# Kernel optimization log

Measured on AMD Instinct MI355X. Metric: run time of the kernel, lower is better.

The kernel has to match this reference:

```python
import jax, jax.numpy as jnp
import numpy as np

GROUPS = 32
EPS = 1e-5

def group_norm(x, scale, bias):
    b, c, h, w = x.shape
    xg = x.reshape(b, GROUPS, c // GROUPS, h, w)
    mean = xg.mean(axis=(2, 3, 4), keepdims=True)
    var = xg.var(axis=(2, 3, 4), keepdims=True)
    xg = (xg - mean) * jax.lax.rsqrt(var + EPS)
    x = xg.reshape(b, c, h, w)
    return x * scale[None, :, None, None] + bias[None, :, None, None]

def conv2d(x, w, b, pad):
    y = jax.lax.conv_general_dilated(
        x, w, window_strides=(1, 1), padding=[(pad, pad), (pad, pad)],
        dimension_numbers=('NCHW', 'OIHW', 'NCHW'))
    return y + b[None, :, None, None]

def setup_inputs() -> dict:
    key = jax.random.key(0)
    ks = jax.random.split(key, 16)
    B, Cin, Cout, H, W, TDIM, NCON = 4, 128, 128, 64, 64, 512, 4
    s = 0.05
    return {
        'x': jax.random.normal(ks[0], (B, Cin, H, W), jnp.float32),
        't': jax.random.normal(ks[1], (B, TDIM), jnp.float32),
        'aim': jax.random.randint(ks[2], (B,), 0, NCON),
        'cond': jax.random.normal(ks[3], (B, Cin, H, W), jnp.float32),
        'gn1_scale': jnp.ones((Cin,), jnp.float32),
        'gn1_bias': jnp.zeros((Cin,), jnp.float32),
        'conv1_w': jax.random.normal(ks[4], (Cout, Cin, 3, 3), jnp.float32) * s,
        'conv1_b': jnp.zeros((Cout,), jnp.float32),
        'mlp_w': jax.random.normal(ks[5], (Cout, TDIM), jnp.float32) * s,
        'mlp_b': jnp.zeros((Cout,), jnp.float32),
        'cond_w': jax.random.normal(ks[6], (Cout, Cin, 1, 1), jnp.float32) * s,
        'cond_b': jnp.zeros((Cout,), jnp.float32),
        'gn2_scale': jnp.ones((Cout,), jnp.float32),
        'gn2_bias': jnp.zeros((Cout,), jnp.float32),
        'conv2_w': jax.random.normal(ks[7], (Cout, Cout, 3, 3), jnp.float32) * s,
        'conv2_b': jnp.zeros((Cout,), jnp.float32),
        'contrast_embed': jax.random.normal(ks[8], (NCON, Cout, 1, 1), jnp.float32),
    }

def reference(x, t, aim, cond, gn1_scale, gn1_bias, conv1_w, conv1_b,
              mlp_w, mlp_b, cond_w, cond_b, gn2_scale, gn2_bias,
              conv2_w, conv2_b, contrast_embed):
    # block1: GN -> SiLU -> 3x3 conv
    h = conv2d(jax.nn.silu(group_norm(x, gn1_scale, gn1_bias)), conv1_w, conv1_b, 1)
    # time embedding: SiLU -> Linear, broadcast over spatial
    temb = jax.nn.silu(t) @ mlp_w.T + mlp_b  # (b, out_ch)
    h = h + temb[:, :, None, None]
    # spatial cross-attention with cond
    c = conv2d(cond, cond_w, cond_b, 0)  # 1x1 projection, (b, C, u, v)
    C = h.shape[1]
    score = jnp.einsum('bchw,bcuv->bhwuv', h, c)  # (b, h, w, u, v)
    # NOTE: softmax over dim=1 (the spatial h axis), as in the source
    score = jax.nn.softmax(score / jnp.sqrt(jnp.float32(C)), axis=1)
    h = h + jnp.einsum('bhwuv,bcuv->bchw', score, c)
    # contrast embedding lookup
    h = h + contrast_embed[aim]  # (b, C, 1, 1) broadcast
    # block2: GN -> SiLU -> (dropout=identity at eval) -> 3x3 conv
    h = conv2d(jax.nn.silu(group_norm(h, gn2_scale, gn2_bias)), conv2_w, conv2_b, 1)
    # res_conv is Identity since in_ch == out_ch
    return h + x
```

## Files before the change

### kernel.cpp

```cpp
#include <hip/hip_runtime.h>
#include <cmath>

#define BB 4
#define CC 128
#define HH 64
#define WW 64
#define SP 4096
#define NG 32
#define TT 64
#define NS 2
#define PSZ ((size_t)BB * SP * CC)

typedef __bf16 bf16x8 __attribute__((ext_vector_type(8)));
typedef __bf16 bf16x4 __attribute__((ext_vector_type(4)));
typedef float  f32x4  __attribute__((ext_vector_type(4)));

__device__ __forceinline__ float silu_f(float v) {
    return v / (1.f + __expf(-v));
}

__device__ __forceinline__ float fast_exp2(float x) {
    return exp2f(x);
}

template<int CTRL>
__device__ __forceinline__ float dpp_add(float v) {
    int m = __builtin_amdgcn_update_dpp(0, __float_as_int(v), CTRL, 0xF, 0xF, true);
    return v + __int_as_float(m);
}
__device__ __forceinline__ float row16_sum(float v) {
    v = dpp_add<0xB1>(v);
    v = dpp_add<0x4E>(v);
    v = dpp_add<0x141>(v);
    v = dpp_add<0x140>(v);
    return v;
}

__global__ __launch_bounds__(256) void prep_kernel(
    const float* __restrict__ x, const float* __restrict__ gn1s,
    const float* __restrict__ gn1b, __bf16* __restrict__ aT,
    const float* __restrict__ c1w, const float* __restrict__ c2w,
    __bf16* __restrict__ wt,
    const float* __restrict__ t, const float* __restrict__ mlpw,
    const float* __restrict__ mlpb, float* __restrict__ tembw,
    const float* __restrict__ cond, const float* __restrict__ cw,
    const float* __restrict__ cb, __bf16* __restrict__ cmT,
    __bf16* __restrict__ cm2, float* __restrict__ gstat)
{
    __shared__ __align__(16) char pool[18432];
    __shared__ float rs[4], rs2[4], mean_s, inv_s;
    const int blk = blockIdx.x;
    const int tid = threadIdx.x;

    if (blk < 128) {
        const int b = blk >> 5, g = blk & 31;
        const float* p = x + (size_t)blk * 16384;
        float s = 0.f, s2 = 0.f;
        for (int it = 0; it < 16; ++it) {
            int q = it * 256 + tid;
            float4 v = *(const float4*)&p[q * 4];
            s += v.x + v.y + v.z + v.w;
            s2 += v.x * v.x + v.y * v.y + v.z * v.z + v.w * v.w;
        }
        #pragma unroll
        for (int off = 32; off >= 1; off >>= 1) {
            s  += __shfl_down(s,  off, 64);
            s2 += __shfl_down(s2, off, 64);
        }
        const int wid = tid >> 6;
        if ((tid & 63) == 0) { rs[wid] = s; rs2[wid] = s2; }
        __syncthreads();
        if (tid == 0) {
            float S = rs[0] + rs[1] + rs[2] + rs[3];
            float S2 = rs2[0] + rs2[1] + rs2[2] + rs2[3];
            float m = S * (1.f / 16384.f);
            float var = S2 * (1.f / 16384.f) - m * m;
            mean_s = m;
            inv_s = rsqrtf(var + 1e-5f);
        }
        __syncthreads();
        const float m = mean_s, inv = inv_s;
        float sc[4], bi[4];
        #pragma unroll
        for (int j = 0; j < 4; ++j) { sc[j] = gn1s[g * 4 + j]; bi[j] = gn1b[g * 4 + j]; }
        for (int it = 0; it < 16; ++it) {
            int pp = it * 256 + tid;
            bf16x4 o;
            #pragma unroll
            for (int j = 0; j < 4; ++j)
                o[j] = (__bf16)silu_f((p[j * 4096 + pp] - m) * inv * sc[j] + bi[j]);
            *(bf16x4*)&aT[((size_t)(b * SP + pp)) * CC + g * 4] = o;
        }
    } else if (blk < 146) {
        const int idx = blk - 128;
        const int wsel = idx / 9, tap = idx % 9;
        const float* src = wsel ? c2w : c1w;
        __bf16* dst = wt + (size_t)wsel * 9 * 16384 + (size_t)tap * 16384;
        for (int it = 0; it < 64; ++it) {
            int q = it * 256 + tid;
            dst[q] = (__bf16)src[(size_t)q * 9 + tap];
        }
    } else if (blk < 154) {
        const int cog = blk - 146;
        float* st = (float*)pool;
        for (int it = 0; it < 8; ++it) {
            int q = it * 256 + tid;
            st[q] = silu_f(t[q]);
        }
        __syncthreads();
        const int col = tid >> 4, seg = tid & 15;
        const float* wr = mlpw + (size_t)(cog * 16 + col) * 512 + seg * 32;
        float acc[4] = {0.f, 0.f, 0.f, 0.f};
        #pragma unroll
        for (int k8 = 0; k8 < 8; ++k8) {
            float4 wv = *(const float4*)&wr[k8 * 4];
            #pragma unroll
            for (int j = 0; j < 4; ++j) {
                int k = seg * 32 + k8 * 4 + j;
                float w4 = (&wv.x)[j];
                acc[0] += st[0 * 512 + k] * w4;
                acc[1] += st[1 * 512 + k] * w4;
                acc[2] += st[2 * 512 + k] * w4;
                acc[3] += st[3 * 512 + k] * w4;
            }
        }
        #pragma unroll
        for (int o = 1; o < 16; o <<= 1) {
            #pragma unroll
            for (int b4 = 0; b4 < 4; ++b4)
                acc[b4] += __shfl_xor(acc[b4], o, 64);
        }
        if (seg == 0) {
            float bv = mlpb[cog * 16 + col];
            #pragma unroll
            for (int b4 = 0; b4 < 4; ++b4)
                tembw[b4 * 128 + cog * 16 + col] = acc[b4] + bv;
        }
    } else if (blk < 410) {
        const int pblk = blk - 154;
        const int b = pblk >> 6;
        const int p0 = (pblk & 63) * 64;
        const int l = tid & 63, wv = tid >> 6;
        const int l15 = l & 15, l4 = l >> 4;
        const int mB = wv * 32;

        __bf16* XT = (__bf16*)pool;

        for (int it = 0; it < 32; ++it) {
            int q = it * 256 + tid;
            float v = cond[((size_t)(b * CC + (q >> 6))) * SP + p0 + (q & 63)];
            XT[(q & 63) * 136 + (q >> 6)] = (__bf16)v;
        }
        __syncthreads();

        f32x4 acc[2][4];
        #pragma unroll
        for (int mb = 0; mb < 2; ++mb)
            #pragma unroll
            for (int nt = 0; nt < 4; ++nt) acc[mb][nt] = (f32x4){0.f, 0.f, 0.f, 0.f};

        #pragma unroll
        for (int ks = 0; ks < 4; ++ks) {
            bf16x8 bfr[4];
            #pragma unroll
            for (int nt = 0; nt < 4; ++nt)
                bfr[nt] = *(const bf16x8*)&XT[(nt * 16 + l15) * 136 + ks * 32 + l4 * 8];
            #pragma unroll
            for (int mb = 0; mb < 2; ++mb) {
                const float* wrow = cw + (size_t)(mB + mb * 16 + l15) * 128 + ks * 32 + l4 * 8;
                float4 wa = *(const float4*)wrow;
                float4 wb4 = *(const float4*)(wrow + 4);
                bf16x8 afr;
                afr[0] = (__bf16)wa.x; afr[1] = (__bf16)wa.y;
                afr[2] = (__bf16)wa.z; afr[3] = (__bf16)wa.w;
                afr[4] = (__bf16)wb4.x; afr[5] = (__bf16)wb4.y;
                afr[6] = (__bf16)wb4.z; afr[7] = (__bf16)wb4.w;
                #pragma unroll
                for (int nt = 0; nt < 4; ++nt)
                    acc[mb][nt] = __builtin_amdgcn_mfma_f32_16x16x32_bf16(afr, bfr[nt], acc[mb][nt], 0, 0, 0);
            }
        }

        const float scl = 0.12751743f;
        #pragma unroll
        for (int mb = 0; mb < 2; ++mb) {
            int co0 = mB + mb * 16 + l4 * 4;
            float bv[4];
            #pragma unroll
            for (int r = 0; r < 4; ++r) bv[r] = cb[co0 + r];
            #pragma unroll
            for (int nt = 0; nt < 4; ++nt) {
                int p = p0 + nt * 16 + l15;
                bf16x4 o;
                #pragma unroll
                for (int r = 0; r < 4; ++r)
                    o[r] = (__bf16)((acc[mb][nt][r] + bv[r]) * scl);
                *(bf16x4*)&cmT[((size_t)(b * SP + p)) * CC + co0] = o;
            }
        }
        __syncthreads();
        __bf16* O2 = (__bf16*)pool;
        #pragma unroll
        for (int mb = 0; mb < 2; ++mb) {
            int co0 = mB + mb * 16 + l4 * 4;
            #pragma unroll
            for (int r = 0; r < 4; ++r) {
                float bv = cb[co0 + r];
                #pragma unroll
                for (int nt = 0; nt < 4; ++nt)
                    O2[(co0 + r) * 72 + nt * 16 + l15] = (__bf16)(acc[mb][nt][r] + bv);
            }
        }
        __syncthreads();
        #pragma unroll
        for (int it = 0; it < 4; ++it) {
            int q = it * 256 + tid;
            int co = q >> 3, pc = q & 7;
            *(bf16x8*)&cm2[((size_t)(b * CC + co)) * SP + p0 + pc * 8] =
                *(const bf16x8*)&O2[co * 72 + pc * 8];
        }
    } else {
        gstat[tid] = 0.f;
    }
}

template<bool FUSE_TEMB, bool OUT_CF, bool FUSE_GN>
__global__ __launch_bounds__(512, 4) void conv_mfma_kernel(
    const __bf16* __restrict__ inT, const __bf16* __restrict__ wt,
    const float* __restrict__ bias, const float* __restrict__ temb,
    const float* __restrict__ resid, __bf16* __restrict__ outT,
    float* __restrict__ outF, const float* __restrict__ gstat,
    const float* __restrict__ gn_s, const float* __restrict__ gn_b)
{
    const int y   = blockIdx.x >> 1;
    const int xh2 = blockIdx.x & 1;
    const int x0  = xh2 * 32;
    const int b   = blockIdx.y;
    const int tid = threadIdx.x;
    const int l = tid & 63, wv = tid >> 6;
    const int l15 = l & 15, l4 = l >> 4;
    const int co_w = wv * 16;

    __shared__ __bf16 inS[3 * 16 * 34 * 8];
    __shared__ float af[128], bfp[128];

    if (FUSE_GN) {
        if (tid < 128) {
            int g = tid >> 2;
            float S = gstat[(b * NG + g) * 2], S2 = gstat[(b * NG + g) * 2 + 1];
            float m = S * (1.f / 16384.f);
            float var = S2 * (1.f / 16384.f) - m * m;
            float inv = rsqrtf(var + 1e-5f);
            float a = inv * gn_s[tid];
            af[tid] = a;
            bfp[tid] = gn_b[tid] - m * a;
        }
        __syncthreads();
    }

    const __bf16* inTb = inT + (size_t)b * SP * CC;
    for (int q = tid; q < 3 * 34 * 16; q += 512) {
        int cc = q & 15;
        int t2 = q >> 4;
        int xs = t2 % 34;
        int r  = t2 / 34;
        int yy = y + r - 1;
        int xg = x0 + xs - 1;
        bf16x8 v;
        if (((unsigned)yy < 64u) && ((unsigned)xg < 64u)) {
            bf16x8 raw = *(const bf16x8*)&inTb[((size_t)(yy * 64 + xg)) * CC + cc * 8];
            if (FUSE_GN) {
                #pragma unroll
                for (int j = 0; j < 8; ++j) {
                    int c = cc * 8 + j;
                    v[j] = (__bf16)silu_f((float)raw[j] * af[c] + bfp[c]);
                }
            } else {
                v = raw;
            }
        } else {
            #pragma unroll
            for (int j = 0; j < 8; ++j) v[j] = (__bf16)0.f;
        }
        *(bf16x8*)&inS[((r * 16 + cc) * 34 + xs) * 8] = v;
    }
    __syncthreads();

    f32x4 acc[2];
    acc[0] = (f32x4){0.f, 0.f, 0.f, 0.f};
    acc[1] = (f32x4){0.f, 0.f, 0.f, 0.f};

    const __bf16* wp = wt + (size_t)(co_w + l15) * 128 + l4 * 8;
    bf16x8 wb[2][4];
    #pragma unroll
    for (int ks = 0; ks < 4; ++ks)
        wb[0][ks] = *(const bf16x8*)(wp + ks * 32);

    #pragma unroll
    for (int tap = 0; tap < 9; ++tap) {
        const int cur = tap & 1, nxt = cur ^ 1;
        if (tap < 8) {
            #pragma unroll
            for (int ks = 0; ks < 4; ++ks)
                wb[nxt][ks] = *(const bf16x8*)(wp + (tap + 1) * 16384 + ks * 32);
        }
        const int rr = tap / 3, dx = tap % 3;
        #pragma unroll
        for (int ks = 0; ks < 4; ++ks) {
            const __bf16* rb = &inS[((rr * 16 + ks * 4 + l4) * 34) * 8];
            bf16x8 b0 = *(const bf16x8*)&rb[(dx + l15) * 8];
            bf16x8 b1 = *(const bf16x8*)&rb[(16 + dx + l15) * 8];
            acc[0] = __builtin_amdgcn_mfma_f32_16x16x32_bf16(wb[cur][ks], b0, acc[0], 0, 0, 0);
            acc[1] = __builtin_amdgcn_mfma_f32_16x16x32_bf16(wb[cur][ks], b1, acc[1], 0, 0, 0);
        }
    }

    if (OUT_CF) {
        #pragma unroll
        for (int r = 0; r < 4; ++r) {
            int co = co_w + l4 * 4 + r;
            float bv = bias[co];
            #pragma unroll
            for (int nb = 0; nb < 2; ++nb) {
                int p = y * 64 + x0 + nb * 16 + l15;
                size_t o = ((size_t)(b * CC + co)) * SP + p;
                outF[o] = acc[nb][r] + bv + resid[o];
            }
        }
    } else {
        int co0 = co_w + l4 * 4;
        float bv[4];
        #pragma unroll
        for (int r = 0; r < 4; ++r)
            bv[r] = bias[co0 + r] + (FUSE_TEMB ? temb[b * CC + co0 + r] : 0.f);
        #pragma unroll
        for (int nb = 0; nb < 2; ++nb) {
            int p = y * 64 + x0 + nb * 16 + l15;
            bf16x4 o;
            #pragma unroll
            for (int r = 0; r < 4; ++r)
                o[r] = (__bf16)(acc[nb][r] + bv[r]);
            *(bf16x4*)&outT[((size_t)(b * SP + p)) * CC + co0] = o;
        }
    }
}

#define CT2 72
#define PBS 72
#define POOL_BYTES 55296
#define NIT (SP / TT / NS)

__global__ __launch_bounds__(512, 4) void attn_kernel(
    const __bf16* __restrict__ h1T, const __bf16* __restrict__ cmT,
    const __bf16* __restrict__ cm2, __bf16* __restrict__ parts)
{
    const int bid = blockIdx.x;
    const int w = bid >> 3;
    const int b = (bid >> 1) & 3;
    const int s = bid & 1;
    const int tid = threadIdx.x;
    const int wid = tid >> 6;
    const int l = tid & 63, l15 = l & 15, l4 = l >> 4;

    __shared__ __align__(16) char pool[POOL_BYTES];
    __bf16* ct2p = (__bf16*)pool;
    __bf16* Pbp  = (__bf16*)(pool + 36864);
    __bf16* Otr  = (__bf16*)pool;

    const __bf16* h1Tb = h1T + (size_t)b * SP * CC;
    const __bf16* cmTb = cmT + (size_t)b * SP * CC;
    const __bf16* cm2b = cm2 + (size_t)b * CC * SP;

    if (wid < 4) {
        const int pw = wid;
        bf16x8 hfr[4][4];
        #pragma unroll
        for (int nt = 0; nt < 4; ++nt)
            #pragma unroll
            for (int ks = 0; ks < 4; ++ks)
                hfr[nt][ks] = *(const bf16x8*)&h1Tb[((size_t)((nt * 16 + l15) * WW + w)) * CC + ks * 32 + l4 * 8];

        bf16x8 afr[4];

        {
            const int uv0 = s * TT;
            const __bf16* arow = cmTb + (size_t)(uv0 + 16 * pw + l15) * CC;
            bf16x8 a0[4];
            #pragma unroll
            for (int ks = 0; ks < 4; ++ks) a0[ks] = *(const bf16x8*)&arow[ks * 32 + l4 * 8];
            f32x4 s1[4];
            __builtin_amdgcn_s_setprio(1);
            #pragma unroll
            for (int nt = 0; nt < 4; ++nt) {
                s1[nt] = (f32x4){0.f, 0.f, 0.f, 0.f};
                #pragma unroll
                for (int ks = 0; ks < 4; ++ks)
                    s1[nt] = __builtin_amdgcn_mfma_f32_16x16x32_bf16(a0[ks], hfr[nt][ks], s1[nt], 0, 0, 0);
            }
            __builtin_amdgcn_s_setprio(0);
            {
                const int uv1 = (NS + s) * TT;
                const __bf16* arow1 = cmTb + (size_t)(uv1 + 16 * pw + l15) * CC;
                #pragma unroll
                for (int ks = 0; ks < 4; ++ks) afr[ks] = *(const bf16x8*)&arow1[ks * 32 + l4 * 8];
            }
            #pragma unroll
            for (int r = 0; r < 4; ++r) {
                float e0 = fast_exp2(s1[0][r]), e1 = fast_exp2(s1[1][r]);
                float e2 = fast_exp2(s1[2][r]), e3 = fast_exp2(s1[3][r]);
                float sm = (e0 + e1) + (e2 + e3);
                sm = row16_sum(sm);
                float ri = 1.f / sm;
                s1[0][r] = e0 * ri; s1[1][r] = e1 * ri;
                s1[2][r] = e2 * ri; s1[3][r] = e3 * ri;
            }
            #pragma unroll
            for (int nt = 0; nt < 4; ++nt) {
                bf16x4 pk;
                pk[0] = (__bf16)s1[nt][0]; pk[1] = (__bf16)s1[nt][1];
                pk[2] = (__bf16)s1[nt][2]; pk[3] = (__bf16)s1[nt][3];
                *(bf16x4*)&Pbp[(nt * 16 + l15) * PBS + 16 * pw + l4 * 4] = pk;
            }
        }
        __syncthreads();

        for (int i = 0; i < NIT; ++i) {
            if (i < NIT - 1) {
                f32x4 s1[4];
                __builtin_amdgcn_s_setprio(1);
                #pragma unroll
                for (int nt = 0; nt < 4; ++nt) {
                    s1[nt] = (f32x4){0.f, 0.f, 0.f, 0.f};
                    #pragma unroll
                    for (int ks = 0; ks < 4; ++ks)
                        s1[nt] = __builtin_amdgcn_mfma_f32_16x16x32_bf16(afr[ks], hfr[nt][ks], s1[nt], 0, 0, 0);
                }
                __builtin_amdgcn_s_setprio(0);
                if (i < NIT - 2) {
                    const int uv2 = ((i + 2) * NS + s) * TT;
                    const __bf16* arow = cmTb + (size_t)(uv2 + 16 * pw + l15) * CC;
                    #pragma unroll
                    for (int ks = 0; ks < 4; ++ks) afr[ks] = *(const bf16x8*)&arow[ks * 32 + l4 * 8];
                }
                #pragma unroll
                for (int r = 0; r < 4; ++r) {
                    float e0 = fast_exp2(s1[0][r]), e1 = fast_exp2(s1[1][r]);
                    float e2 = fast_exp2(s1[2][r]), e3 = fast_exp2(s1[3][r]);
                    float sm = (e0 + e1) + (e2 + e3);
                    sm = row16_sum(sm);
                    float ri = 1.f / sm;
                    s1[0][r] = e0 * ri; s1[1][r] = e1 * ri;
                    s1[2][r] = e2 * ri; s1[3][r] = e3 * ri;
                }
                __bf16* PbW = Pbp + ((i & 1) ^ 1) * 4608;
                #pragma unroll
                for (int nt = 0; nt < 4; ++nt) {
                    bf16x4 pk;
                    pk[0] = (__bf16)s1[nt][0]; pk[1] = (__bf16)s1[nt][1];
                    pk[2] = (__bf16)s1[nt][2]; pk[3] = (__bf16)s1[nt][3];
                    *(bf16x4*)&PbW[(nt * 16 + l15) * PBS + 16 * pw + l4 * 4] = pk;
                }
            }
            __syncthreads();
        }
    } else {
        const int cw = wid - 4;
        const int hB = (cw & 1) * 32;
        const int cB = (cw >> 1) * 64;
        const int tc = tid - 256;
        const int sc = tc >> 3;
        const int stc = tc & 7;

        f32x4 acc2[2][4];
        #pragma unroll
        for (int mb = 0; mb < 2; ++mb)
            #pragma unroll
            for (int nt = 0; nt < 4; ++nt) acc2[mb][nt] = (f32x4){0.f, 0.f, 0.f, 0.f};

        bf16x8 st4[4];

        {
            const int uv0 = s * TT;
            #pragma unroll
            for (int it = 0; it < 4; ++it) {
                int c = it * 32 + sc;
                *(bf16x8*)&ct2p[c * CT2 + stc * 8] =
                    *(const bf16x8*)&cm2b[(size_t)c * SP + uv0 + stc * 8];
            }
            const int uv1 = (NS + s) * TT;
            #pragma unroll
            for (int it = 0; it < 4; ++it) {
                int c = it * 32 + sc;
                st4[it] = *(const bf16x8*)&cm2b[(size_t)c * SP + uv1 + stc * 8];
            }
        }
        __syncthreads();

        for (int i = 0; i < NIT; ++i) {
            const int cur = i & 1;
            {
                const __bf16* PbR = Pbp + cur * 4608;
                const __bf16* ctR = ct2p + cur * 9216;
                bf16x8 pfr[2][2];
                #pragma unroll
                for (int mb = 0; mb < 2; ++mb)
                    #pragma unroll
                    for (int ks = 0; ks < 2; ++ks)
                        pfr[mb][ks] = *(const bf16x8*)&PbR[(hB + mb * 16 + l15) * PBS + ks * 32 + l4 * 8];
                bf16x8 bfr[4][2];
                #pragma unroll
                for (int nt = 0; nt < 4; ++nt)
                    #pragma unroll
                    for (int ks = 0; ks < 2; ++ks)
                        bfr[nt][ks] = *(const bf16x8*)&ctR[(cB + nt * 16 + l15) * CT2 + ks * 32 + l4 * 8];
                __builtin_amdgcn_s_setprio(1);
                #pragma unroll
                for (int mb = 0; mb < 2; ++mb)
                    #pragma unroll
                    for (int nt = 0; nt < 4; ++nt)
                        #pragma unroll
                        for (int ks = 0; ks < 2; ++ks)
                            acc2[mb][nt] = __builtin_amdgcn_mfma_f32_16x16x32_bf16(
                                pfr[mb][ks], bfr[nt][ks], acc2[mb][nt], 0, 0, 0);
                __builtin_amdgcn_s_setprio(0);
            }
            if (i < NIT - 1) {
                __bf16* ctW = ct2p + (cur ^ 1) * 9216;
                #pragma unroll
                for (int it = 0; it < 4; ++it) {
                    int c = it * 32 + sc;
                    *(bf16x8*)&ctW[c * CT2 + stc * 8] = st4[it];
                }
                if (i < NIT - 2) {
                    const int uv2 = ((i + 2) * NS + s) * TT;
                    #pragma unroll
                    for (int it = 0; it < 4; ++it) {
                        int c = it * 32 + sc;
                        st4[it] = *(const bf16x8*)&cm2b[(size_t)c * SP + uv2 + stc * 8];
                    }
                }
            }
            __syncthreads();
        }

        #pragma unroll
        for (int mb = 0; mb < 2; ++mb)
            #pragma unroll
            for (int nt = 0; nt < 4; ++nt)
                #pragma unroll
                for (int r = 0; r < 4; ++r)
                    Otr[(hB + mb * 16 + l4 * 4 + r) * 136 + cB + nt * 16 + l15] =
                        (__bf16)acc2[mb][nt][r];
    }

    __syncthreads();
    __bf16* pO = parts + (size_t)s * PSZ;
    #pragma unroll
    for (int it = 0; it < 2; ++it) {
        int q = it * 512 + tid;
        int h = q >> 4, cc = q & 15;
        *(bf16x8*)&pO[((size_t)(b * SP + h * WW + w)) * CC + cc * 8] =
            *(const bf16x8*)&Otr[h * 136 + cc * 8];
    }
}

__global__ __launch_bounds__(256) void gn2_stats_kernel(
    const __bf16* __restrict__ h1T, const __bf16* __restrict__ parts,
    const int* __restrict__ aim, const float* __restrict__ emb,
    __bf16* __restrict__ h2T, float* __restrict__ gstat)
{
    const int pb = blockIdx.x, b = blockIdx.y;
    const int tid = threadIdx.x;
    const int c8 = tid & 15, rw = tid >> 4;
    const float4 ev0 = *(const float4*)&emb[aim[b] * CC + c8 * 8];
    const float4 ev1 = *(const float4*)&emb[aim[b] * CC + c8 * 8 + 4];
    float sa = 0.f, s2a = 0.f, sb = 0.f, s2b = 0.f;
    #pragma unroll
    for (int it = 0; it < 2; ++it) {
        int prow = pb * 32 + it * 16 + rw;
        size_t base = ((size_t)(b * SP + prow)) * CC + c8 * 8;
        bf16x8 hv = *(const bf16x8*)&h1T[base];
        bf16x8 a0 = *(const bf16x8*)&parts[base];
        bf16x8 a1 = *(const bf16x8*)&parts[PSZ + base];
        float v[8];
        #pragma unroll
        for (int j = 0; j < 4; ++j)
            v[j] = (float)hv[j] + (&ev0.x)[j] + (float)a0[j] + (float)a1[j];
        #pragma unroll
        for (int j = 4; j < 8; ++j)
            v[j] = (float)hv[j] + (&ev1.x)[j - 4] + (float)a0[j] + (float)a1[j];
        bf16x8 o;
        #pragma unroll
        for (int j = 0; j < 8; ++j) o[j] = (__bf16)v[j];
        *(bf16x8*)&h2T[base] = o;
        #pragma unroll
        for (int j = 0; j < 4; ++j) { sa += v[j]; s2a += v[j] * v[j]; }
        #pragma unroll
        for (int j = 4; j < 8; ++j) { sb += v[j]; s2b += v[j] * v[j]; }
    }
    sa  += __shfl_xor(sa,  16, 64); sa  += __shfl_xor(sa,  32, 64);
    s2a += __shfl_xor(s2a, 16, 64); s2a += __shfl_xor(s2a, 32, 64);
    sb  += __shfl_xor(sb,  16, 64); sb  += __shfl_xor(sb,  32, 64);
    s2b += __shfl_xor(s2b, 16, 64); s2b += __shfl_xor(s2b, 32, 64);
    __shared__ float ls[4][16][4];
    const int wv = tid >> 6;
    if ((tid & 63) < 16) {
        ls[wv][c8][0] = sa;  ls[wv][c8][1] = s2a;
        ls[wv][c8][2] = sb;  ls[wv][c8][3] = s2b;
    }
    __syncthreads();
    if (tid < 16) {
        float A = 0.f, A2 = 0.f, Bs = 0.f, B2 = 0.f;
        #pragma unroll
        for (int v2 = 0; v2 < 4; ++v2) {
            A  += ls[v2][tid][0]; A2 += ls[v2][tid][1];
            Bs += ls[v2][tid][2]; B2 += ls[v2][tid][3];
        }
        atomicAdd(&gstat[(b * NG + tid * 2) * 2],     A);
        atomicAdd(&gstat[(b * NG + tid * 2) * 2 + 1], A2);
        atomicAdd(&gstat[(b * NG + tid * 2 + 1) * 2],     Bs);
        atomicAdd(&gstat[(b * NG + tid * 2 + 1) * 2 + 1], B2);
    }
}

extern "C" void kernel_launch(void* const* d_in, const int* in_sizes, int n_in,
                              void* d_out, int out_size, void* d_ws, size_t ws_size,
                              hipStream_t stream)
{
    const float* x     = (const float*)d_in[0];
    const float* t     = (const float*)d_in[1];
    const int*   aim   = (const int*)  d_in[2];
    const float* cond  = (const float*)d_in[3];
    const float* gn1s  = (const float*)d_in[4];
    const float* gn1b  = (const float*)d_in[5];
    const float* c1w   = (const float*)d_in[6];
    const float* c1b   = (const float*)d_in[7];
    const float* mlpw  = (const float*)d_in[8];
    const float* mlpb  = (const float*)d_in[9];
    const float* cw    = (const float*)d_in[10];
    const float* cb    = (const float*)d_in[11];
    const float* gn2s  = (const float*)d_in[12];
    const float* gn2b  = (const float*)d_in[13];
    const float* c2w   = (const float*)d_in[14];
    const float* c2b   = (const float*)d_in[15];
    const float* emb   = (const float*)d_in[16];
    float* out = (float*)d_out;
    float* ws = (float*)d_ws;

    __bf16* aT    = (__bf16*)ws;
    __bf16* h1T   = (__bf16*)(ws + 1048576);
    __bf16* cmT   = (__bf16*)(ws + 2097152);
    __bf16* cm2   = (__bf16*)(ws + 3145728);
    __bf16* parts = (__bf16*)(ws + 4194304);
    __bf16* wt    = (__bf16*)(ws + 6291456);
    float*  tembw = ws + 6438912;
    float*  gstat = ws + 6439424;
    __bf16* h2T   = cmT;

    prep_kernel<<<dim3(411), dim3(256), 0, stream>>>(
        x, gn1s, gn1b, aT, c1w, c2w, wt, t, mlpw, mlpb, tembw,
        cond, cw, cb, cmT, cm2, gstat);
    conv_mfma_kernel<true, false, false><<<dim3(128, BB), dim3(512), 0, stream>>>(
        aT, wt, c1b, tembw, nullptr, h1T, nullptr, nullptr, nullptr, nullptr);
    attn_kernel<<<dim3(WW * BB * NS), dim3(512), 0, stream>>>(h1T, cmT, cm2, parts);
    gn2_stats_kernel<<<dim3(128, BB), dim3(256), 0, stream>>>(h1T, parts, aim, emb, h2T, gstat);
    conv_mfma_kernel<false, true, true><<<dim3(128, BB), dim3(512), 0, stream>>>(
        h2T, wt + (size_t)9 * 16384, c2b, nullptr, x, nullptr, out, gstat, gn2s, gn2b);
}
```

Measured before the change: 215.4 us.

## Fuse split-K attention partial reduction and GN2 stats into attention kernel

Merges the two uv-split halves of each attention column into one 1024-thread block, so the partial outputs stay in LDS and are combined on-chip instead of going through a global parts buffer. The residual add, contrast embedding, h2T write and GN2 group-stat atomics move into the attention epilogue, which removes the separate gn2_stats kernel and its global round trip. The cost is half as many blocks, doubled LDS per block (about 110KB) which lowers occupancy, and block-wide __syncthreads now spanning both split groups.

```diff
diff --git a/kernel.cpp b/kernel.cpp
--- a/kernel.cpp
+++ b/kernel.cpp
@@ -347,32 +347,37 @@
 
 #define CT2 72
 #define PBS 72
-#define POOL_BYTES 55296
+#define PIPE_BYTES 55296
 #define NIT (SP / TT / NS)
 
-__global__ __launch_bounds__(512, 4) void attn_kernel(
+__global__ __launch_bounds__(1024, 4) void attn_kernel(
     const __bf16* __restrict__ h1T, const __bf16* __restrict__ cmT,
-    const __bf16* __restrict__ cm2, __bf16* __restrict__ parts)
+    const __bf16* __restrict__ cm2, __bf16* __restrict__ h2T,
+    const int* __restrict__ aim, const float* __restrict__ emb,
+    float* __restrict__ gstat)
 {
     const int bid = blockIdx.x;
-    const int w = bid >> 3;
-    const int b = (bid >> 1) & 3;
-    const int s = bid & 1;
+    const int b = bid & 3;
+    const int w = bid >> 2;
     const int tid = threadIdx.x;
     const int wid = tid >> 6;
+    const int sg  = wid >> 3;
+    const int wl  = wid & 7;
     const int l = tid & 63, l15 = l & 15, l4 = l >> 4;
-
-    __shared__ __align__(16) char pool[POOL_BYTES];
-    __bf16* ct2p = (__bf16*)pool;
-    __bf16* Pbp  = (__bf16*)(pool + 36864);
-    __bf16* Otr  = (__bf16*)pool;
+    const int s = sg;
+
+    __shared__ __align__(16) char pool[2 * PIPE_BYTES];
+    __shared__ float ls[16][16][4];
+    char* base = pool + sg * PIPE_BYTES;
+    __bf16* ct2p = (__bf16*)base;
+    __bf16* Pbp  = (__bf16*)(base + 36864);
 
     const __bf16* h1Tb = h1T + (size_t)b * SP * CC;
     const __bf16* cmTb = cmT + (size_t)b * SP * CC;
     const __bf16* cm2b = cm2 + (size_t)b * CC * SP;
 
-    if (wid < 4) {
-        const int pw = wid;
+    if (wl < 4) {
+        const int pw = wl;
         bf16x8 hfr[4][4];
         #pragma unroll
         for (int nt = 0; nt < 4; ++nt)
@@ -464,10 +469,10 @@
             __syncthreads();
         }
     } else {
-        const int cw = wid - 4;
+        const int cw = wl - 4;
         const int hB = (cw & 1) * 32;
         const int cB = (cw >> 1) * 64;
-        const int tc = tid - 256;
+        const int tc = tid & 255;
         const int sc = tc >> 3;
         const int stc = tc & 7;
 
@@ -543,6 +548,7 @@
             __syncthreads();
         }
 
+        __bf16* Otr = (__bf16*)base;
         #pragma unroll
         for (int mb = 0; mb < 2; ++mb)
             #pragma unroll
@@ -554,72 +560,50 @@
     }
 
     __syncthreads();
-    __bf16* pO = parts + (size_t)s * PSZ;
-    #pragma unroll
-    for (int it = 0; it < 2; ++it) {
-        int q = it * 512 + tid;
-        int h = q >> 4, cc = q & 15;
-        *(bf16x8*)&pO[((size_t)(b * SP + h * WW + w)) * CC + cc * 8] =
-            *(const bf16x8*)&Otr[h * 136 + cc * 8];
-    }
-}
-
-__global__ __launch_bounds__(256) void gn2_stats_kernel(
-    const __bf16* __restrict__ h1T, const __bf16* __restrict__ parts,
-    const int* __restrict__ aim, const float* __restrict__ emb,
-    __bf16* __restrict__ h2T, float* __restrict__ gstat)
-{
-    const int pb = blockIdx.x, b = blockIdx.y;
-    const int tid = threadIdx.x;
-    const int c8 = tid & 15, rw = tid >> 4;
-    const float4 ev0 = *(const float4*)&emb[aim[b] * CC + c8 * 8];
-    const float4 ev1 = *(const float4*)&emb[aim[b] * CC + c8 * 8 + 4];
-    float sa = 0.f, s2a = 0.f, sb = 0.f, s2b = 0.f;
-    #pragma unroll
-    for (int it = 0; it < 2; ++it) {
-        int prow = pb * 32 + it * 16 + rw;
-        size_t base = ((size_t)(b * SP + prow)) * CC + c8 * 8;
-        bf16x8 hv = *(const bf16x8*)&h1T[base];
-        bf16x8 a0 = *(const bf16x8*)&parts[base];
-        bf16x8 a1 = *(const bf16x8*)&parts[PSZ + base];
+    {
+        const __bf16* Otr0 = (const __bf16*)pool;
+        const __bf16* Otr1 = (const __bf16*)(pool + PIPE_BYTES);
+        const int h = tid >> 4, cc = tid & 15;
+        const int off = h * 136 + cc * 8;
+        bf16x8 o0 = *(const bf16x8*)&Otr0[off];
+        bf16x8 o1 = *(const bf16x8*)&Otr1[off];
+        size_t gbase = ((size_t)(b * SP + h * WW + w)) * CC + cc * 8;
+        bf16x8 hv = *(const bf16x8*)&h1T[gbase];
+        const float4 ev0 = *(const float4*)&emb[aim[b] * CC + cc * 8];
+        const float4 ev1 = *(const float4*)&emb[aim[b] * CC + cc * 8 + 4];
         float v[8];
         #pragma unroll
         for (int j = 0; j < 4; ++j)
-            v[j] = (float)hv[j] + (&ev0.x)[j] + (float)a0[j] + (float)a1[j];
+            v[j] = (float)hv[j] + (float)o0[j] + (float)o1[j] + (&ev0.x)[j];
         #pragma unroll
         for (int j = 4; j < 8; ++j)
-            v[j] = (float)hv[j] + (&ev1.x)[j - 4] + (float)a0[j] + (float)a1[j];
-        bf16x8 o;
-        #pragma unroll
-        for (int j = 0; j < 8; ++j) o[j] = (__bf16)v[j];
-        *(bf16x8*)&h2T[base] = o;
+            v[j] = (float)hv[j] + (float)o0[j] + (float)o1[j] + (&ev1.x)[j - 4];
+        bf16x8 ov;
+        #pragma unroll
+        for (int j = 0; j < 8; ++j) ov[j] = (__bf16)v[j];
+        *(bf16x8*)&h2T[gbase] = ov;
+        float sa = 0.f, s2a = 0.f, sb = 0.f, s2b = 0.f;
         #pragma unroll
         for (int j = 0; j < 4; ++j) { sa += v[j]; s2a += v[j] * v[j]; }
         #pragma unroll
         for (int j = 4; j < 8; ++j) { sb += v[j]; s2b += v[j] * v[j]; }
-    }
-    sa  += __shfl_xor(sa,  16, 64); sa  += __shfl_xor(sa,  32, 64);
-    s2a += __shfl_xor(s2a, 16, 64); s2a += __shfl_xor(s2a, 32, 64);
-    sb  += __shfl_xor(sb,  16, 64); sb  += __shfl_xor(sb,  32, 64);
-    s2b += __shfl_xor(s2b, 16, 64); s2b += __shfl_xor(s2b, 32, 64);
-    __shared__ float ls[4][16][4];
-    const int wv = tid >> 6;
-    if ((tid & 63) < 16) {
-        ls[wv][c8][0] = sa;  ls[wv][c8][1] = s2a;
-        ls[wv][c8][2] = sb;  ls[wv][c8][3] = s2b;
+        sa  += __shfl_xor(sa,  16, 64); sa  += __shfl_xor(sa,  32, 64);
+        s2a += __shfl_xor(s2a, 16, 64); s2a += __shfl_xor(s2a, 32, 64);
+        sb  += __shfl_xor(sb,  16, 64); sb  += __shfl_xor(sb,  32, 64);
+        s2b += __shfl_xor(s2b, 16, 64); s2b += __shfl_xor(s2b, 32, 64);
+        if (l < 16) {
+            ls[wid][l][0] = sa;  ls[wid][l][1] = s2a;
+            ls[wid][l][2] = sb;  ls[wid][l][3] = s2b;
+        }
     }
     __syncthreads();
-    if (tid < 16) {
-        float A = 0.f, A2 = 0.f, Bs = 0.f, B2 = 0.f;
-        #pragma unroll
-        for (int v2 = 0; v2 < 4; ++v2) {
-            A  += ls[v2][tid][0]; A2 += ls[v2][tid][1];
-            Bs += ls[v2][tid][2]; B2 += ls[v2][tid][3];
-        }
-        atomicAdd(&gstat[(b * NG + tid * 2) * 2],     A);
-        atomicAdd(&gstat[(b * NG + tid * 2) * 2 + 1], A2);
-        atomicAdd(&gstat[(b * NG + tid * 2 + 1) * 2],     Bs);
-        atomicAdd(&gstat[(b * NG + tid * 2 + 1) * 2 + 1], B2);
+    if (tid < 64) {
+        const int cc = tid & 15, k = tid >> 4;
+        float v = 0.f;
+        #pragma unroll
+        for (int wv = 0; wv < 16; ++wv) v += ls[wv][cc][k];
+        const int g = cc * 2 + (k >> 1);
+        atomicAdd(&gstat[(b * NG + g) * 2 + (k & 1)], v);
     }
 }
 
@@ -651,19 +635,18 @@
     __bf16* h1T   = (__bf16*)(ws + 1048576);
     __bf16* cmT   = (__bf16*)(ws + 2097152);
     __bf16* cm2   = (__bf16*)(ws + 3145728);
-    __bf16* parts = (__bf16*)(ws + 4194304);
+    __bf16* h2T   = (__bf16*)(ws + 4194304);
     __bf16* wt    = (__bf16*)(ws + 6291456);
     float*  tembw = ws + 6438912;
     float*  gstat = ws + 6439424;
-    __bf16* h2T   = cmT;
 
     prep_kernel<<<dim3(411), dim3(256), 0, stream>>>(
         x, gn1s, gn1b, aT, c1w, c2w, wt, t, mlpw, mlpb, tembw,
         cond, cw, cb, cmT, cm2, gstat);
     conv_mfma_kernel<true, false, false><<<dim3(128, BB), dim3(512), 0, stream>>>(
         aT, wt, c1b, tembw, nullptr, h1T, nullptr, nullptr, nullptr, nullptr);
-    attn_kernel<<<dim3(WW * BB * NS), dim3(512), 0, stream>>>(h1T, cmT, cm2, parts);
-    gn2_stats_kernel<<<dim3(128, BB), dim3(256), 0, stream>>>(h1T, parts, aim, emb, h2T, gstat);
+    attn_kernel<<<dim3(WW * BB), dim3(1024), 0, stream>>>(
+        h1T, cmT, cm2, h2T, aim, emb, gstat);
     conv_mfma_kernel<false, true, true><<<dim3(128, BB), dim3(512), 0, stream>>>(
         h2T, wt + (size_t)9 * 16384, c2b, nullptr, x, nullptr, out, gstat, gn2s, gn2b);
 }
```

After: 199.4 us. -7.5%, faster.
